# Kernel tuning notes

Hardware: AMD Instinct MI355X
Metric: run time of the kernel (lower is better)

Reference implementation:

```python
import jax, jax.numpy as jnp
import numpy as np

D_MODEL = 128
N_HEADS = 4
HEAD_DIM = D_MODEL // N_HEADS


def setup_inputs() -> dict:
    key = jax.random.key(0)
    kx, kq, ko = jax.random.split(key, 3)
    B, T = 4, 4096
    x = jax.random.normal(kx, (B, T, D_MODEL), dtype=jnp.float32)
    s = 1.0 / np.sqrt(D_MODEL)
    # torch nn.Linear weight: [out, in]; y = x @ W.T
    W_qkv = jax.random.uniform(kq, (3 * D_MODEL, D_MODEL), dtype=jnp.float32, minval=-s, maxval=s)
    W_out = jax.random.uniform(ko, (D_MODEL, D_MODEL), dtype=jnp.float32, minval=-s, maxval=s)
    return {"x": x, "W_qkv": W_qkv, "W_out": W_out}


def reference(x, W_qkv, W_out):
    B, T, _ = x.shape
    qkv = (x @ W_qkv.T).reshape(B, T, 3, N_HEADS, HEAD_DIM)
    q, k, v = qkv[:, :, 0], qkv[:, :, 1], qkv[:, :, 2]  # [B,T,H,D]
    # scores: [B,H,T,T]
    scores = jnp.einsum('bthd,bshd->bhts', q, k) / jnp.sqrt(jnp.float32(HEAD_DIM))
    causal = jnp.triu(jnp.ones((T, T), dtype=bool), 1)
    scores = jnp.where(causal, -jnp.inf, scores)
    attn = jax.nn.softmax(scores, axis=-1)
    out = jnp.einsum('bhts,bshd->bthd', attn, v).reshape(B, T, D_MODEL)
    return out @ W_out.T
```

## Files before the change

kernel.cpp:

```cpp
#include <hip/hip_runtime.h>
#include <math.h>

#define B_   4
#define T_   4096
#define DM_  128
#define NH_  4
#define HD_  32
#define TOKENS (B_ * T_)

typedef __attribute__((ext_vector_type(8))) short short8;
typedef __attribute__((ext_vector_type(4))) float floatx4;

__device__ __forceinline__ unsigned short f2bf(float f) {
    union { float f; unsigned int u; } v; v.f = f;
    unsigned int u = v.u;
    u += 0x7fffu + ((u >> 16) & 1u);
    return (unsigned short)(u >> 16);
}
__device__ __forceinline__ void split_bf(float v, unsigned short& hi, unsigned short& lo) {
    unsigned short h = f2bf(v);
    float hf = __uint_as_float(((unsigned int)h) << 16);
    hi = h;
    lo = f2bf(v - hf);
}

#define LROW 136

__global__ __launch_bounds__(256) void qkv_proj_kernel(
    const float* __restrict__ x, const float* __restrict__ Wqkv,
    unsigned short* __restrict__ q_bf, unsigned short* __restrict__ k_bf,
    unsigned short* __restrict__ v_t)
{
    __shared__ __align__(16) unsigned short whi[64 * LROW];
    __shared__ __align__(16) unsigned short wlo[64 * LROW];

    const int tid  = threadIdx.x;
    const int wave = tid >> 6, lane = tid & 63;
    const int m    = lane & 15, q4 = lane >> 4;
    const int m0   = blockIdx.x * 64;
    const int ch   = blockIdx.y;
    const float scale = 0.2550052509571414f;

    {
        const float4* wg = (const float4*)(Wqkv + (size_t)ch * 64 * DM_);
        #pragma unroll
        for (int i = 0; i < 8; ++i) {
            const int f = tid + 256 * i;
            float4 v = wg[f];
            const int row = f >> 5, k4 = f & 31;
            ushort4 h, l;
            split_bf(v.x, h.x, l.x); split_bf(v.y, h.y, l.y);
            split_bf(v.z, h.z, l.z); split_bf(v.w, h.w, l.w);
            *(ushort4*)(whi + row * LROW + k4 * 4) = h;
            *(ushort4*)(wlo + row * LROW + k4 * 4) = l;
        }
    }

    short8 Ah[4], Al[4];
    {
        const float4* xg = (const float4*)(x + (size_t)(m0 + wave * 16 + m) * DM_);
        #pragma unroll
        for (int ks = 0; ks < 4; ++ks) {
            float4 a = xg[ks * 8 + q4 * 2];
            float4 b = xg[ks * 8 + q4 * 2 + 1];
            ushort4 h0, l0, h1, l1;
            split_bf(a.x, h0.x, l0.x); split_bf(a.y, h0.y, l0.y);
            split_bf(a.z, h0.z, l0.z); split_bf(a.w, h0.w, l0.w);
            split_bf(b.x, h1.x, l1.x); split_bf(b.y, h1.y, l1.y);
            split_bf(b.z, h1.z, l1.z); split_bf(b.w, h1.w, l1.w);
            Ah[ks] = short8{(short)h0.x, (short)h0.y, (short)h0.z, (short)h0.w,
                            (short)h1.x, (short)h1.y, (short)h1.z, (short)h1.w};
            Al[ks] = short8{(short)l0.x, (short)l0.y, (short)l0.z, (short)l0.w,
                            (short)l1.x, (short)l1.y, (short)l1.z, (short)l1.w};
        }
    }
    __syncthreads();

    #pragma unroll
    for (int nb = 0; nb < 4; ++nb) {
        floatx4 acc = {0.f, 0.f, 0.f, 0.f};
        #pragma unroll
        for (int ks = 0; ks < 4; ++ks) {
            short8 Bh = *(const short8*)(whi + (nb * 16 + m) * LROW + ks * 32 + q4 * 8);
            short8 Bl = *(const short8*)(wlo + (nb * 16 + m) * LROW + ks * 32 + q4 * 8);
            acc = __builtin_amdgcn_mfma_f32_16x16x32_bf16(Ah[ks], Bh, acc, 0, 0, 0);
            acc = __builtin_amdgcn_mfma_f32_16x16x32_bf16(Ah[ks], Bl, acc, 0, 0, 0);
            acc = __builtin_amdgcn_mfma_f32_16x16x32_bf16(Al[ks], Bh, acc, 0, 0, 0);
        }
        const int n    = ch * 64 + nb * 16 + m;
        const int cidx = n >> 7;
        const int hh   = (n >> 5) & 3;
        const int d    = n & 31;
        const int tok0 = m0 + wave * 16 + q4 * 4;
        const int b    = tok0 >> 12;
        const int t0   = tok0 & (T_ - 1);
        const int bh   = b * NH_ + hh;
        if (cidx == 0) {
            #pragma unroll
            for (int reg = 0; reg < 4; ++reg)
                q_bf[((size_t)bh * T_ + t0 + reg) * HD_ + d] = f2bf(acc[reg] * scale);
        } else if (cidx == 1) {
            #pragma unroll
            for (int reg = 0; reg < 4; ++reg)
                k_bf[((size_t)bh * T_ + t0 + reg) * HD_ + d] = f2bf(acc[reg]);
        } else {
            ushort4 p;
            p.x = f2bf(acc[0]); p.y = f2bf(acc[1]);
            p.z = f2bf(acc[2]); p.w = f2bf(acc[3]);
            *(ushort4*)(v_t + ((size_t)bh * HD_ + d) * T_ + t0) = p;
        }
    }
}

__global__ __launch_bounds__(256, 4) void attn_mfma_kernel(
    const unsigned short* __restrict__ qb, const unsigned short* __restrict__ kb,
    const unsigned short* __restrict__ vtb, float* __restrict__ og)
{
    __shared__ __align__(16) char smem[5120 + 4608 + 4 * 2304];
    char* kLds = smem;
    char* vLds = smem + 5120;
    const int tid  = threadIdx.x;
    const int wave = tid >> 6, lane = tid & 63;
    const int m    = lane & 15, q4 = lane >> 4;
    char* pT = smem + 9728 + wave * 2304;

    const int pid = blockIdx.x;
    const int xcd = pid & 7;
    const int r_  = pid >> 3;
    const int bh  = xcd * 2 + (r_ & 1);
    const int j_  = r_ >> 1;
    const int a_  = j_ & 15, k_ = j_ >> 4;
    const int qt  = (k_ == 0) ? a_ : (k_ == 1) ? 63 - a_
                  : (k_ == 2) ? 32 + a_ : 31 - a_;

    const size_t qkbase = (size_t)bh * T_ * HD_;
    const char* kg = (const char*)(kb + qkbase);
    const char* vg = (const char*)(vtb + qkbase);

    short8 qf = *(const short8*)((const char*)(qb + qkbase)
                 + (size_t)(qt * 64 + wave * 16 + m) * 64 + q4 * 16);
    const int qrow = wave * 16 + m;

    floatx4 O0 = {0.f, 0.f, 0.f, 0.f}, O1 = {0.f, 0.f, 0.f, 0.f};
    float mx = -INFINITY, ls = 0.f;

    for (int kt = 0; kt <= qt; ++kt) {
        __syncthreads();
        {
            const int krow = tid >> 2, ku = tid & 3;
            short8 kv = *(const short8*)(kg + (size_t)(kt * 64 + krow) * 64 + ku * 16);
            const int vd = tid >> 3, vu = tid & 7;
            short8 vv = *(const short8*)(vg + (size_t)vd * (T_ * 2)
                                            + (size_t)kt * 128 + vu * 16);
            *(short8*)(kLds + krow * 80 + ku * 16) = kv;
            *(short8*)(vLds + vd * 144 + vu * 16) = vv;
        }
        __syncthreads();

        floatx4 st[4];
        #pragma unroll
        for (int sb = 0; sb < 4; ++sb) {
            short8 kfrag = *(const short8*)(kLds + (sb * 16 + m) * 80 + q4 * 16);
            floatx4 z = {0.f, 0.f, 0.f, 0.f};
            st[sb] = __builtin_amdgcn_mfma_f32_16x16x32_bf16(kfrag, qf, z, 0, 0, 0);
        }

        if (kt == qt) {
            #pragma unroll
            for (int sb = 0; sb < 4; ++sb)
                #pragma unroll
                for (int reg = 0; reg < 4; ++reg)
                    if (sb * 16 + q4 * 4 + reg > qrow) st[sb][reg] = -INFINITY;
        }

        float rmax = -INFINITY;
        #pragma unroll
        for (int sb = 0; sb < 4; ++sb)
            #pragma unroll
            for (int reg = 0; reg < 4; ++reg) rmax = fmaxf(rmax, st[sb][reg]);
        rmax = fmaxf(rmax, __shfl_xor(rmax, 16, 64));
        rmax = fmaxf(rmax, __shfl_xor(rmax, 32, 64));

        const float mn = fmaxf(mx, rmax);
        const float alpha = __builtin_amdgcn_exp2f(mx - mn);
        mx = mn;

        float psum = 0.f;
        #pragma unroll
        for (int sb = 0; sb < 4; ++sb) {
            float p0 = __builtin_amdgcn_exp2f(st[sb][0] - mn);
            float p1 = __builtin_amdgcn_exp2f(st[sb][1] - mn);
            float p2 = __builtin_amdgcn_exp2f(st[sb][2] - mn);
            float p3 = __builtin_amdgcn_exp2f(st[sb][3] - mn);
            psum += (p0 + p1) + (p2 + p3);
            unsigned u0 = __float_as_uint(p0) + 0x8000u;
            unsigned u1 = __float_as_uint(p1) + 0x8000u;
            unsigned u2 = __float_as_uint(p2) + 0x8000u;
            unsigned u3 = __float_as_uint(p3) + 0x8000u;
            uint2 pk;
            pk.x = __builtin_amdgcn_perm(u1, u0, 0x07060302);
            pk.y = __builtin_amdgcn_perm(u3, u2, 0x07060302);
            *(uint2*)(pT + m * 144 + sb * 32 + q4 * 8) = pk;
        }
        psum += __shfl_xor(psum, 16, 64);
        psum += __shfl_xor(psum, 32, 64);
        ls = ls * alpha + psum;
        #pragma unroll
        for (int reg = 0; reg < 4; ++reg) { O0[reg] *= alpha; O1[reg] *= alpha; }

        __asm__ volatile("s_waitcnt lgkmcnt(0)" ::: "memory");

        short8 b0  = *(const short8*)(pT + m * 144 + q4 * 16);
        short8 b1  = *(const short8*)(pT + m * 144 + 64 + q4 * 16);
        short8 v00 = *(const short8*)(vLds + m * 144 + q4 * 16);
        short8 v10 = *(const short8*)(vLds + m * 144 + 64 + q4 * 16);
        short8 v01 = *(const short8*)(vLds + (16 + m) * 144 + q4 * 16);
        short8 v11 = *(const short8*)(vLds + (16 + m) * 144 + 64 + q4 * 16);
        O0 = __builtin_amdgcn_mfma_f32_16x16x32_bf16(v00, b0, O0, 0, 0, 0);
        O0 = __builtin_amdgcn_mfma_f32_16x16x32_bf16(v10, b1, O0, 0, 0, 0);
        O1 = __builtin_amdgcn_mfma_f32_16x16x32_bf16(v01, b0, O1, 0, 0, 0);
        O1 = __builtin_amdgcn_mfma_f32_16x16x32_bf16(v11, b1, O1, 0, 0, 0);
    }

    const float inv = 1.f / ls;
    const int b = bh >> 2, h = bh & 3;
    const int t = qt * 64 + qrow;
    float* orow = og + (((size_t)b * T_ + t) * NH_ + h) * HD_;
    *(float4*)(orow + q4 * 4)      = make_float4(O0[0] * inv, O0[1] * inv,
                                                 O0[2] * inv, O0[3] * inv);
    *(float4*)(orow + 16 + q4 * 4) = make_float4(O1[0] * inv, O1[1] * inv,
                                                 O1[2] * inv, O1[3] * inv);
}

__global__ __launch_bounds__(256) void out_proj_kernel(
    const float* __restrict__ a, const float* __restrict__ Wout,
    float* __restrict__ out)
{
    __shared__ __align__(16) unsigned short whi[64 * LROW];
    __shared__ __align__(16) unsigned short wlo[64 * LROW];

    const int tid  = threadIdx.x;
    const int wave = tid >> 6, lane = tid & 63;
    const int m    = lane & 15, q4 = lane >> 4;
    const int m0   = blockIdx.x * 64;
    const int ch   = blockIdx.y;

    {
        const float4* wg = (const float4*)(Wout + (size_t)ch * 64 * DM_);
        #pragma unroll
        for (int i = 0; i < 8; ++i) {
            const int f = tid + 256 * i;
            float4 v = wg[f];
            const int row = f >> 5, k4 = f & 31;
            ushort4 h, l;
            split_bf(v.x, h.x, l.x); split_bf(v.y, h.y, l.y);
            split_bf(v.z, h.z, l.z); split_bf(v.w, h.w, l.w);
            *(ushort4*)(whi + row * LROW + k4 * 4) = h;
            *(ushort4*)(wlo + row * LROW + k4 * 4) = l;
        }
    }

    short8 Ah[4], Al[4];
    {
        const float4* xg = (const float4*)(a + (size_t)(m0 + wave * 16 + m) * DM_);
        #pragma unroll
        for (int ks = 0; ks < 4; ++ks) {
            float4 av = xg[ks * 8 + q4 * 2];
            float4 bv = xg[ks * 8 + q4 * 2 + 1];
            ushort4 h0, l0, h1, l1;
            split_bf(av.x, h0.x, l0.x); split_bf(av.y, h0.y, l0.y);
            split_bf(av.z, h0.z, l0.z); split_bf(av.w, h0.w, l0.w);
            split_bf(bv.x, h1.x, l1.x); split_bf(bv.y, h1.y, l1.y);
            split_bf(bv.z, h1.z, l1.z); split_bf(bv.w, h1.w, l1.w);
            Ah[ks] = short8{(short)h0.x, (short)h0.y, (short)h0.z, (short)h0.w,
                            (short)h1.x, (short)h1.y, (short)h1.z, (short)h1.w};
            Al[ks] = short8{(short)l0.x, (short)l0.y, (short)l0.z, (short)l0.w,
                            (short)l1.x, (short)l1.y, (short)l1.z, (short)l1.w};
        }
    }
    __syncthreads();

    #pragma unroll
    for (int nb = 0; nb < 4; ++nb) {
        floatx4 acc = {0.f, 0.f, 0.f, 0.f};
        #pragma unroll
        for (int ks = 0; ks < 4; ++ks) {
            short8 Bh = *(const short8*)(whi + (nb * 16 + m) * LROW + ks * 32 + q4 * 8);
            short8 Bl = *(const short8*)(wlo + (nb * 16 + m) * LROW + ks * 32 + q4 * 8);
            acc = __builtin_amdgcn_mfma_f32_16x16x32_bf16(Ah[ks], Bh, acc, 0, 0, 0);
            acc = __builtin_amdgcn_mfma_f32_16x16x32_bf16(Ah[ks], Bl, acc, 0, 0, 0);
            acc = __builtin_amdgcn_mfma_f32_16x16x32_bf16(Al[ks], Bh, acc, 0, 0, 0);
        }
        const int n = ch * 64 + nb * 16 + m;
        const int tok0 = m0 + wave * 16 + q4 * 4;
        #pragma unroll
        for (int reg = 0; reg < 4; ++reg)
            out[(size_t)(tok0 + reg) * DM_ + n] = acc[reg];
    }
}

extern "C" void kernel_launch(void* const* d_in, const int* in_sizes, int n_in,
                              void* d_out, int out_size, void* d_ws, size_t ws_size,
                              hipStream_t stream) {
    const float* x    = (const float*)d_in[0];
    const float* Wqkv = (const float*)d_in[1];
    const float* Wout = (const float*)d_in[2];
    float* out = (float*)d_out;

    char* ws = (char*)d_ws;
    unsigned short* q_bf  = (unsigned short*)(ws);
    unsigned short* k_bf  = (unsigned short*)(ws + (size_t)4 * 1024 * 1024);
    unsigned short* v_t   = (unsigned short*)(ws + (size_t)8 * 1024 * 1024);
    float*          att_ws = (float*)(ws + (size_t)12 * 1024 * 1024);

    qkv_proj_kernel<<<dim3(TOKENS / 64, 6), 256, 0, stream>>>(x, Wqkv, q_bf, k_bf, v_t);
    attn_mfma_kernel<<<1024, 256, 0, stream>>>(q_bf, k_bf, v_t, att_ws);
    out_proj_kernel<<<dim3(TOKENS / 64, 2), 256, 0, stream>>>(att_ws, Wout, out);
}
```

Baseline: 146.8 us.

## Give each attention wave its own 32-row query tile and drop shared K/V staging

The attention kernel now assigns each wave an independent 32-row query tile, with the four waves of a block taking mirrored tiles to balance the causal work. K and V fragments are loaded straight from global memory into registers, which removes LDS staging and the per-iteration block barriers. The row sum is computed with an extra MFMA against a ones vector instead of shuffle reductions, and the grid is halved. The V projection also swaps its MFMA operand order so V^T is written along contiguous tokens. Possible downsides are extra global/L2 traffic, since K/V are no longer shared across waves, and higher register pressure.

Result: slower. 161.4 us (+10.0%).

```diff
diff --git a/kernel.cpp b/kernel.cpp
--- a/kernel.cpp
+++ b/kernel.cpp
@@ -76,160 +76,197 @@
     }
     __syncthreads();
 
-    #pragma unroll
-    for (int nb = 0; nb < 4; ++nb) {
-        floatx4 acc = {0.f, 0.f, 0.f, 0.f};
-        #pragma unroll
-        for (int ks = 0; ks < 4; ++ks) {
-            short8 Bh = *(const short8*)(whi + (nb * 16 + m) * LROW + ks * 32 + q4 * 8);
-            short8 Bl = *(const short8*)(wlo + (nb * 16 + m) * LROW + ks * 32 + q4 * 8);
-            acc = __builtin_amdgcn_mfma_f32_16x16x32_bf16(Ah[ks], Bh, acc, 0, 0, 0);
-            acc = __builtin_amdgcn_mfma_f32_16x16x32_bf16(Ah[ks], Bl, acc, 0, 0, 0);
-            acc = __builtin_amdgcn_mfma_f32_16x16x32_bf16(Al[ks], Bh, acc, 0, 0, 0);
-        }
-        const int n    = ch * 64 + nb * 16 + m;
-        const int cidx = n >> 7;
-        const int hh   = (n >> 5) & 3;
-        const int d    = n & 31;
-        const int tok0 = m0 + wave * 16 + q4 * 4;
-        const int b    = tok0 >> 12;
-        const int t0   = tok0 & (T_ - 1);
-        const int bh   = b * NH_ + hh;
-        if (cidx == 0) {
-            #pragma unroll
-            for (int reg = 0; reg < 4; ++reg)
-                q_bf[((size_t)bh * T_ + t0 + reg) * HD_ + d] = f2bf(acc[reg] * scale);
-        } else if (cidx == 1) {
-            #pragma unroll
-            for (int reg = 0; reg < 4; ++reg)
-                k_bf[((size_t)bh * T_ + t0 + reg) * HD_ + d] = f2bf(acc[reg]);
-        } else {
-            ushort4 p;
-            p.x = f2bf(acc[0]); p.y = f2bf(acc[1]);
-            p.z = f2bf(acc[2]); p.w = f2bf(acc[3]);
-            *(ushort4*)(v_t + ((size_t)bh * HD_ + d) * T_ + t0) = p;
-        }
-    }
-}
-
-__global__ __launch_bounds__(256, 4) void attn_mfma_kernel(
+    const int b    = m0 >> 12;
+    const int tloc = (m0 & (T_ - 1)) + wave * 16;
+
+    if (ch < 4) {
+        #pragma unroll
+        for (int nb = 0; nb < 4; ++nb) {
+            floatx4 acc = {0.f, 0.f, 0.f, 0.f};
+            #pragma unroll
+            for (int ks = 0; ks < 4; ++ks) {
+                short8 Bh = *(const short8*)(whi + (nb * 16 + m) * LROW + ks * 32 + q4 * 8);
+                short8 Bl = *(const short8*)(wlo + (nb * 16 + m) * LROW + ks * 32 + q4 * 8);
+                acc = __builtin_amdgcn_mfma_f32_16x16x32_bf16(Ah[ks], Bh, acc, 0, 0, 0);
+                acc = __builtin_amdgcn_mfma_f32_16x16x32_bf16(Ah[ks], Bl, acc, 0, 0, 0);
+                acc = __builtin_amdgcn_mfma_f32_16x16x32_bf16(Al[ks], Bh, acc, 0, 0, 0);
+            }
+            const int n  = ch * 64 + nb * 16 + m;
+            const int hh = (n >> 5) & 3;
+            const int d  = n & 31;
+            const int bh = b * NH_ + hh;
+            const int t0 = tloc + q4 * 4;
+            if (ch < 2) {
+                #pragma unroll
+                for (int reg = 0; reg < 4; ++reg)
+                    q_bf[((size_t)bh * T_ + t0 + reg) * HD_ + d] = f2bf(acc[reg] * scale);
+            } else {
+                #pragma unroll
+                for (int reg = 0; reg < 4; ++reg)
+                    k_bf[((size_t)bh * T_ + t0 + reg) * HD_ + d] = f2bf(acc[reg]);
+            }
+        }
+    } else {
+        #pragma unroll
+        for (int nb = 0; nb < 4; ++nb) {
+            floatx4 acc = {0.f, 0.f, 0.f, 0.f};
+            #pragma unroll
+            for (int ks = 0; ks < 4; ++ks) {
+                short8 Bh = *(const short8*)(whi + (nb * 16 + m) * LROW + ks * 32 + q4 * 8);
+                short8 Bl = *(const short8*)(wlo + (nb * 16 + m) * LROW + ks * 32 + q4 * 8);
+                acc = __builtin_amdgcn_mfma_f32_16x16x32_bf16(Bh, Ah[ks], acc, 0, 0, 0);
+                acc = __builtin_amdgcn_mfma_f32_16x16x32_bf16(Bh, Al[ks], acc, 0, 0, 0);
+                acc = __builtin_amdgcn_mfma_f32_16x16x32_bf16(Bl, Ah[ks], acc, 0, 0, 0);
+            }
+            const int t = tloc + m;
+            #pragma unroll
+            for (int reg = 0; reg < 4; ++reg) {
+                const int n  = ch * 64 + nb * 16 + q4 * 4 + reg;
+                const int hh = (n >> 5) & 3;
+                const int d  = n & 31;
+                v_t[((size_t)(b * NH_ + hh) * HD_ + d) * T_ + t] = f2bf(acc[reg]);
+            }
+        }
+    }
+}
+
+__global__ __launch_bounds__(256) void attn_mfma_kernel(
     const unsigned short* __restrict__ qb, const unsigned short* __restrict__ kb,
     const unsigned short* __restrict__ vtb, float* __restrict__ og)
 {
-    __shared__ __align__(16) char smem[5120 + 4608 + 4 * 2304];
-    char* kLds = smem;
-    char* vLds = smem + 5120;
+    __shared__ __align__(16) char pSm[4 * 32 * 144];
     const int tid  = threadIdx.x;
     const int wave = tid >> 6, lane = tid & 63;
     const int m    = lane & 15, q4 = lane >> 4;
-    char* pT = smem + 9728 + wave * 2304;
-
-    const int pid = blockIdx.x;
-    const int xcd = pid & 7;
-    const int r_  = pid >> 3;
-    const int bh  = xcd * 2 + (r_ & 1);
-    const int j_  = r_ >> 1;
-    const int a_  = j_ & 15, k_ = j_ >> 4;
-    const int qt  = (k_ == 0) ? a_ : (k_ == 1) ? 63 - a_
-                  : (k_ == 2) ? 32 + a_ : 31 - a_;
+    char* pT = pSm + wave * 4608;
+
+    const int bidx = blockIdx.x;
+    const int xcd  = bidx & 7;
+    const int g    = bidx >> 3;
+    const int bh   = xcd * 2 + (g & 1);
+    const int u    = g >> 1;
+    const int qt   = (wave == 0) ? u : (wave == 1) ? 127 - u
+                   : (wave == 2) ? 64 + u : 63 - u;
 
     const size_t qkbase = (size_t)bh * T_ * HD_;
     const char* kg = (const char*)(kb + qkbase);
     const char* vg = (const char*)(vtb + qkbase);
-
-    short8 qf = *(const short8*)((const char*)(qb + qkbase)
-                 + (size_t)(qt * 64 + wave * 16 + m) * 64 + q4 * 16);
-    const int qrow = wave * 16 + m;
-
-    floatx4 O0 = {0.f, 0.f, 0.f, 0.f}, O1 = {0.f, 0.f, 0.f, 0.f};
-    float mx = -INFINITY, ls = 0.f;
-
-    for (int kt = 0; kt <= qt; ++kt) {
-        __syncthreads();
-        {
-            const int krow = tid >> 2, ku = tid & 3;
-            short8 kv = *(const short8*)(kg + (size_t)(kt * 64 + krow) * 64 + ku * 16);
-            const int vd = tid >> 3, vu = tid & 7;
-            short8 vv = *(const short8*)(vg + (size_t)vd * (T_ * 2)
-                                            + (size_t)kt * 128 + vu * 16);
-            *(short8*)(kLds + krow * 80 + ku * 16) = kv;
-            *(short8*)(vLds + vd * 144 + vu * 16) = vv;
-        }
-        __syncthreads();
-
-        floatx4 st[4];
-        #pragma unroll
-        for (int sb = 0; sb < 4; ++sb) {
-            short8 kfrag = *(const short8*)(kLds + (sb * 16 + m) * 80 + q4 * 16);
-            floatx4 z = {0.f, 0.f, 0.f, 0.f};
-            st[sb] = __builtin_amdgcn_mfma_f32_16x16x32_bf16(kfrag, qf, z, 0, 0, 0);
-        }
-
-        if (kt == qt) {
+    const char* qg = (const char*)(qb + qkbase);
+
+    short8 qf[2];
+    #pragma unroll
+    for (int qb_ = 0; qb_ < 2; ++qb_)
+        qf[qb_] = *(const short8*)(qg + (size_t)(qt * 32 + qb_ * 16 + m) * 64 + q4 * 16);
+
+    const short ob = (short)0x3F80;
+    const short8 onesf = (m == 0) ? short8{ob, ob, ob, ob, ob, ob, ob, ob}
+                                  : short8{0, 0, 0, 0, 0, 0, 0, 0};
+
+    floatx4 O[2][2] = {{{0.f,0.f,0.f,0.f},{0.f,0.f,0.f,0.f}},
+                       {{0.f,0.f,0.f,0.f},{0.f,0.f,0.f,0.f}}};
+    floatx4 Cs[2] = {{0.f,0.f,0.f,0.f},{0.f,0.f,0.f,0.f}};
+    float mx[2] = {-INFINITY, -INFINITY};
+
+    const int ktN = (qt * 32 + 31) >> 6;
+
+    for (int kt = 0; kt <= ktN; ++kt) {
+        short8 kf[4];
+        #pragma unroll
+        for (int sb = 0; sb < 4; ++sb)
+            kf[sb] = *(const short8*)(kg + (size_t)(kt * 64 + sb * 16 + m) * 64 + q4 * 16);
+        short8 vf[2][2];
+        #pragma unroll
+        for (int db = 0; db < 2; ++db)
+            #pragma unroll
+            for (int h = 0; h < 2; ++h)
+                vf[db][h] = *(const short8*)(vg + (size_t)(db * 16 + m) * (T_ * 2)
+                                                + kt * 128 + h * 64 + q4 * 16);
+
+        floatx4 st[4][2];
+        #pragma unroll
+        for (int sb = 0; sb < 4; ++sb)
+            #pragma unroll
+            for (int qb_ = 0; qb_ < 2; ++qb_) {
+                floatx4 z = {0.f, 0.f, 0.f, 0.f};
+                st[sb][qb_] = __builtin_amdgcn_mfma_f32_16x16x32_bf16(kf[sb], qf[qb_], z, 0, 0, 0);
+            }
+
+        if (kt == ktN) {
             #pragma unroll
             for (int sb = 0; sb < 4; ++sb)
                 #pragma unroll
-                for (int reg = 0; reg < 4; ++reg)
-                    if (sb * 16 + q4 * 4 + reg > qrow) st[sb][reg] = -INFINITY;
-        }
-
-        float rmax = -INFINITY;
-        #pragma unroll
-        for (int sb = 0; sb < 4; ++sb)
-            #pragma unroll
-            for (int reg = 0; reg < 4; ++reg) rmax = fmaxf(rmax, st[sb][reg]);
-        rmax = fmaxf(rmax, __shfl_xor(rmax, 16, 64));
-        rmax = fmaxf(rmax, __shfl_xor(rmax, 32, 64));
-
-        const float mn = fmaxf(mx, rmax);
-        const float alpha = __builtin_amdgcn_exp2f(mx - mn);
-        mx = mn;
-
-        float psum = 0.f;
-        #pragma unroll
-        for (int sb = 0; sb < 4; ++sb) {
-            float p0 = __builtin_amdgcn_exp2f(st[sb][0] - mn);
-            float p1 = __builtin_amdgcn_exp2f(st[sb][1] - mn);
-            float p2 = __builtin_amdgcn_exp2f(st[sb][2] - mn);
-            float p3 = __builtin_amdgcn_exp2f(st[sb][3] - mn);
-            psum += (p0 + p1) + (p2 + p3);
-            unsigned u0 = __float_as_uint(p0) + 0x8000u;
-            unsigned u1 = __float_as_uint(p1) + 0x8000u;
-            unsigned u2 = __float_as_uint(p2) + 0x8000u;
-            unsigned u3 = __float_as_uint(p3) + 0x8000u;
-            uint2 pk;
-            pk.x = __builtin_amdgcn_perm(u1, u0, 0x07060302);
-            pk.y = __builtin_amdgcn_perm(u3, u2, 0x07060302);
-            *(uint2*)(pT + m * 144 + sb * 32 + q4 * 8) = pk;
-        }
-        psum += __shfl_xor(psum, 16, 64);
-        psum += __shfl_xor(psum, 32, 64);
-        ls = ls * alpha + psum;
-        #pragma unroll
-        for (int reg = 0; reg < 4; ++reg) { O0[reg] *= alpha; O1[reg] *= alpha; }
+                for (int qb_ = 0; qb_ < 2; ++qb_) {
+                    const int qloc = ((qt & 1) << 5) + qb_ * 16 + m;
+                    #pragma unroll
+                    for (int reg = 0; reg < 4; ++reg)
+                        if (sb * 16 + q4 * 4 + reg > qloc) st[sb][qb_][reg] = -INFINITY;
+                }
+        }
+
+        #pragma unroll
+        for (int qb_ = 0; qb_ < 2; ++qb_) {
+            float rmax = -INFINITY;
+            #pragma unroll
+            for (int sb = 0; sb < 4; ++sb)
+                #pragma unroll
+                for (int reg = 0; reg < 4; ++reg) rmax = fmaxf(rmax, st[sb][qb_][reg]);
+            rmax = fmaxf(rmax, __shfl_xor(rmax, 16, 64));
+            rmax = fmaxf(rmax, __shfl_xor(rmax, 32, 64));
+            const float mn = fmaxf(mx[qb_], rmax);
+            const float alpha = __builtin_amdgcn_exp2f(mx[qb_] - mn);
+            mx[qb_] = mn;
+            #pragma unroll
+            for (int db = 0; db < 2; ++db)
+                #pragma unroll
+                for (int reg = 0; reg < 4; ++reg) O[db][qb_][reg] *= alpha;
+            #pragma unroll
+            for (int reg = 0; reg < 4; ++reg) Cs[qb_][reg] *= alpha;
+
+            #pragma unroll
+            for (int sb = 0; sb < 4; ++sb) {
+                float p0 = __builtin_amdgcn_exp2f(st[sb][qb_][0] - mn);
+                float p1 = __builtin_amdgcn_exp2f(st[sb][qb_][1] - mn);
+                float p2 = __builtin_amdgcn_exp2f(st[sb][qb_][2] - mn);
+                float p3 = __builtin_amdgcn_exp2f(st[sb][qb_][3] - mn);
+                unsigned u0 = __float_as_uint(p0) + 0x8000u;
+                unsigned u1 = __float_as_uint(p1) + 0x8000u;
+                unsigned u2 = __float_as_uint(p2) + 0x8000u;
+                unsigned u3 = __float_as_uint(p3) + 0x8000u;
+                uint2 pk;
+                pk.x = __builtin_amdgcn_perm(u1, u0, 0x07060302);
+                pk.y = __builtin_amdgcn_perm(u3, u2, 0x07060302);
+                *(uint2*)(pT + (qb_ * 16 + m) * 144 + sb * 32 + q4 * 8) = pk;
+            }
+        }
 
         __asm__ volatile("s_waitcnt lgkmcnt(0)" ::: "memory");
 
-        short8 b0  = *(const short8*)(pT + m * 144 + q4 * 16);
-        short8 b1  = *(const short8*)(pT + m * 144 + 64 + q4 * 16);
-        short8 v00 = *(const short8*)(vLds + m * 144 + q4 * 16);
-        short8 v10 = *(const short8*)(vLds + m * 144 + 64 + q4 * 16);
-        short8 v01 = *(const short8*)(vLds + (16 + m) * 144 + q4 * 16);
-        short8 v11 = *(const short8*)(vLds + (16 + m) * 144 + 64 + q4 * 16);
-        O0 = __builtin_amdgcn_mfma_f32_16x16x32_bf16(v00, b0, O0, 0, 0, 0);
-        O0 = __builtin_amdgcn_mfma_f32_16x16x32_bf16(v10, b1, O0, 0, 0, 0);
-        O1 = __builtin_amdgcn_mfma_f32_16x16x32_bf16(v01, b0, O1, 0, 0, 0);
-        O1 = __builtin_amdgcn_mfma_f32_16x16x32_bf16(v11, b1, O1, 0, 0, 0);
-    }
-
-    const float inv = 1.f / ls;
+        #pragma unroll
+        for (int qb_ = 0; qb_ < 2; ++qb_) {
+            short8 pf0 = *(const short8*)(pT + (qb_ * 16 + m) * 144 + q4 * 16);
+            short8 pf1 = *(const short8*)(pT + (qb_ * 16 + m) * 144 + 64 + q4 * 16);
+            O[0][qb_] = __builtin_amdgcn_mfma_f32_16x16x32_bf16(vf[0][0], pf0, O[0][qb_], 0, 0, 0);
+            O[0][qb_] = __builtin_amdgcn_mfma_f32_16x16x32_bf16(vf[0][1], pf1, O[0][qb_], 0, 0, 0);
+            O[1][qb_] = __builtin_amdgcn_mfma_f32_16x16x32_bf16(vf[1][0], pf0, O[1][qb_], 0, 0, 0);
+            O[1][qb_] = __builtin_amdgcn_mfma_f32_16x16x32_bf16(vf[1][1], pf1, O[1][qb_], 0, 0, 0);
+            Cs[qb_]   = __builtin_amdgcn_mfma_f32_16x16x32_bf16(onesf, pf0, Cs[qb_], 0, 0, 0);
+            Cs[qb_]   = __builtin_amdgcn_mfma_f32_16x16x32_bf16(onesf, pf1, Cs[qb_], 0, 0, 0);
+        }
+    }
+
     const int b = bh >> 2, h = bh & 3;
-    const int t = qt * 64 + qrow;
-    float* orow = og + (((size_t)b * T_ + t) * NH_ + h) * HD_;
-    *(float4*)(orow + q4 * 4)      = make_float4(O0[0] * inv, O0[1] * inv,
-                                                 O0[2] * inv, O0[3] * inv);
-    *(float4*)(orow + 16 + q4 * 4) = make_float4(O1[0] * inv, O1[1] * inv,
-                                                 O1[2] * inv, O1[3] * inv);
+    #pragma unroll
+    for (int qb_ = 0; qb_ < 2; ++qb_) {
+        const float l = __shfl(Cs[qb_][0], m, 64);
+        const float inv = 1.f / l;
+        const int t = qt * 32 + qb_ * 16 + m;
+        float* orow = og + (((size_t)b * T_ + t) * NH_ + h) * HD_;
+        #pragma unroll
+        for (int db = 0; db < 2; ++db)
+            *(float4*)(orow + db * 16 + q4 * 4) =
+                make_float4(O[db][qb_][0] * inv, O[db][qb_][1] * inv,
+                            O[db][qb_][2] * inv, O[db][qb_][3] * inv);
+    }
 }
 
 __global__ __launch_bounds__(256) void out_proj_kernel(
@@ -314,6 +351,6 @@
     float*          att_ws = (float*)(ws + (size_t)12 * 1024 * 1024);
 
     qkv_proj_kernel<<<dim3(TOKENS / 64, 6), 256, 0, stream>>>(x, Wqkv, q_bf, k_bf, v_t);
-    attn_mfma_kernel<<<1024, 256, 0, stream>>>(q_bf, k_bf, v_t, att_ws);
+    attn_mfma_kernel<<<512, 256, 0, stream>>>(q_bf, k_bf, v_t, att_ws);
     out_proj_kernel<<<dim3(TOKENS / 64, 2), 256, 0, stream>>>(att_ws, Wout, out);
 }
```

## Pre-split weights once and emit attention output as bf16 hi/lo pairs

Applied to the files above, without the earlier changes.

Adds a small kernel that splits both weight matrices into bf16 hi/lo parts once, so the projection kernels stop redoing the split per block through LDS and can drop the block-wide sync. The attention kernel now writes its output already split into hi/lo bf16 planes, and the output projection loads these directly instead of converting fp32. The V projection path also swaps MFMA operand order, so each lane writes tokens contiguously into the transposed V layout. The cost is an extra kernel launch and weight fragments read from global/L2 instead of LDS.

Result: slower. 171.6 us (+16.9%).

```diff
diff --git a/kernel.cpp b/kernel.cpp
--- a/kernel.cpp
+++ b/kernel.cpp
@@ -24,37 +24,36 @@
     lo = f2bf(v - hf);
 }
 
-#define LROW 136
+__global__ __launch_bounds__(256) void w_split_kernel(
+    const float* __restrict__ Wqkv, const float* __restrict__ Wout,
+    unsigned short* __restrict__ w_hi, unsigned short* __restrict__ w_lo,
+    unsigned short* __restrict__ wo_hi, unsigned short* __restrict__ wo_lo)
+{
+    const int i = blockIdx.x * 256 + threadIdx.x;
+    {
+        unsigned short h, l;
+        split_bf(Wqkv[i], h, l);
+        w_hi[i] = h; w_lo[i] = l;
+    }
+    if (i < DM_ * DM_) {
+        unsigned short h, l;
+        split_bf(Wout[i], h, l);
+        wo_hi[i] = h; wo_lo[i] = l;
+    }
+}
 
 __global__ __launch_bounds__(256) void qkv_proj_kernel(
-    const float* __restrict__ x, const float* __restrict__ Wqkv,
+    const float* __restrict__ x,
+    const unsigned short* __restrict__ w_hi, const unsigned short* __restrict__ w_lo,
     unsigned short* __restrict__ q_bf, unsigned short* __restrict__ k_bf,
     unsigned short* __restrict__ v_t)
 {
-    __shared__ __align__(16) unsigned short whi[64 * LROW];
-    __shared__ __align__(16) unsigned short wlo[64 * LROW];
-
     const int tid  = threadIdx.x;
     const int wave = tid >> 6, lane = tid & 63;
     const int m    = lane & 15, q4 = lane >> 4;
     const int m0   = blockIdx.x * 64;
     const int ch   = blockIdx.y;
     const float scale = 0.2550052509571414f;
-
-    {
-        const float4* wg = (const float4*)(Wqkv + (size_t)ch * 64 * DM_);
-        #pragma unroll
-        for (int i = 0; i < 8; ++i) {
-            const int f = tid + 256 * i;
-            float4 v = wg[f];
-            const int row = f >> 5, k4 = f & 31;
-            ushort4 h, l;
-            split_bf(v.x, h.x, l.x); split_bf(v.y, h.y, l.y);
-            split_bf(v.z, h.z, l.z); split_bf(v.w, h.w, l.w);
-            *(ushort4*)(whi + row * LROW + k4 * 4) = h;
-            *(ushort4*)(wlo + row * LROW + k4 * 4) = l;
-        }
-    }
 
     short8 Ah[4], Al[4];
     {
@@ -74,47 +73,67 @@
                             (short)l1.x, (short)l1.y, (short)l1.z, (short)l1.w};
         }
     }
-    __syncthreads();
-
-    #pragma unroll
-    for (int nb = 0; nb < 4; ++nb) {
-        floatx4 acc = {0.f, 0.f, 0.f, 0.f};
-        #pragma unroll
-        for (int ks = 0; ks < 4; ++ks) {
-            short8 Bh = *(const short8*)(whi + (nb * 16 + m) * LROW + ks * 32 + q4 * 8);
-            short8 Bl = *(const short8*)(wlo + (nb * 16 + m) * LROW + ks * 32 + q4 * 8);
-            acc = __builtin_amdgcn_mfma_f32_16x16x32_bf16(Ah[ks], Bh, acc, 0, 0, 0);
-            acc = __builtin_amdgcn_mfma_f32_16x16x32_bf16(Ah[ks], Bl, acc, 0, 0, 0);
-            acc = __builtin_amdgcn_mfma_f32_16x16x32_bf16(Al[ks], Bh, acc, 0, 0, 0);
-        }
-        const int n    = ch * 64 + nb * 16 + m;
-        const int cidx = n >> 7;
-        const int hh   = (n >> 5) & 3;
-        const int d    = n & 31;
-        const int tok0 = m0 + wave * 16 + q4 * 4;
-        const int b    = tok0 >> 12;
-        const int t0   = tok0 & (T_ - 1);
-        const int bh   = b * NH_ + hh;
-        if (cidx == 0) {
-            #pragma unroll
-            for (int reg = 0; reg < 4; ++reg)
-                q_bf[((size_t)bh * T_ + t0 + reg) * HD_ + d] = f2bf(acc[reg] * scale);
-        } else if (cidx == 1) {
-            #pragma unroll
-            for (int reg = 0; reg < 4; ++reg)
-                k_bf[((size_t)bh * T_ + t0 + reg) * HD_ + d] = f2bf(acc[reg]);
-        } else {
-            ushort4 p;
-            p.x = f2bf(acc[0]); p.y = f2bf(acc[1]);
-            p.z = f2bf(acc[2]); p.w = f2bf(acc[3]);
-            *(ushort4*)(v_t + ((size_t)bh * HD_ + d) * T_ + t0) = p;
+
+    const unsigned short* wh = w_hi + (size_t)ch * 64 * DM_;
+    const unsigned short* wl = w_lo + (size_t)ch * 64 * DM_;
+    const int b    = m0 >> 12;
+    const int tloc = (m0 & (T_ - 1)) + wave * 16;
+
+    if (ch < 4) {
+        #pragma unroll
+        for (int nb = 0; nb < 4; ++nb) {
+            floatx4 acc = {0.f, 0.f, 0.f, 0.f};
+            #pragma unroll
+            for (int ks = 0; ks < 4; ++ks) {
+                short8 Bh = *(const short8*)(wh + (nb * 16 + m) * DM_ + ks * 32 + q4 * 8);
+                short8 Bl = *(const short8*)(wl + (nb * 16 + m) * DM_ + ks * 32 + q4 * 8);
+                acc = __builtin_amdgcn_mfma_f32_16x16x32_bf16(Ah[ks], Bh, acc, 0, 0, 0);
+                acc = __builtin_amdgcn_mfma_f32_16x16x32_bf16(Ah[ks], Bl, acc, 0, 0, 0);
+                acc = __builtin_amdgcn_mfma_f32_16x16x32_bf16(Al[ks], Bh, acc, 0, 0, 0);
+            }
+            const int n  = ch * 64 + nb * 16 + m;
+            const int hh = (n >> 5) & 3;
+            const int d  = n & 31;
+            const int bh = b * NH_ + hh;
+            const int t0 = tloc + q4 * 4;
+            if (ch < 2) {
+                #pragma unroll
+                for (int reg = 0; reg < 4; ++reg)
+                    q_bf[((size_t)bh * T_ + t0 + reg) * HD_ + d] = f2bf(acc[reg] * scale);
+            } else {
+                #pragma unroll
+                for (int reg = 0; reg < 4; ++reg)
+                    k_bf[((size_t)bh * T_ + t0 + reg) * HD_ + d] = f2bf(acc[reg]);
+            }
+        }
+    } else {
+        #pragma unroll
+        for (int nb = 0; nb < 4; ++nb) {
+            floatx4 acc = {0.f, 0.f, 0.f, 0.f};
+            #pragma unroll
+            for (int ks = 0; ks < 4; ++ks) {
+                short8 Bh = *(const short8*)(wh + (nb * 16 + m) * DM_ + ks * 32 + q4 * 8);
+                short8 Bl = *(const short8*)(wl + (nb * 16 + m) * DM_ + ks * 32 + q4 * 8);
+                acc = __builtin_amdgcn_mfma_f32_16x16x32_bf16(Bh, Ah[ks], acc, 0, 0, 0);
+                acc = __builtin_amdgcn_mfma_f32_16x16x32_bf16(Bh, Al[ks], acc, 0, 0, 0);
+                acc = __builtin_amdgcn_mfma_f32_16x16x32_bf16(Bl, Ah[ks], acc, 0, 0, 0);
+            }
+            const int t = tloc + m;
+            #pragma unroll
+            for (int reg = 0; reg < 4; ++reg) {
+                const int n  = ch * 64 + nb * 16 + q4 * 4 + reg;
+                const int hh = (n >> 5) & 3;
+                const int d  = n & 31;
+                v_t[((size_t)(b * NH_ + hh) * HD_ + d) * T_ + t] = f2bf(acc[reg]);
+            }
         }
     }
 }
 
 __global__ __launch_bounds__(256, 4) void attn_mfma_kernel(
     const unsigned short* __restrict__ qb, const unsigned short* __restrict__ kb,
-    const unsigned short* __restrict__ vtb, float* __restrict__ og)
+    const unsigned short* __restrict__ vtb,
+    unsigned short* __restrict__ att_hi, unsigned short* __restrict__ att_lo)
 {
     __shared__ __align__(16) char smem[5120 + 4608 + 4 * 2304];
     char* kLds = smem;
@@ -225,68 +244,49 @@
     const float inv = 1.f / ls;
     const int b = bh >> 2, h = bh & 3;
     const int t = qt * 64 + qrow;
-    float* orow = og + (((size_t)b * T_ + t) * NH_ + h) * HD_;
-    *(float4*)(orow + q4 * 4)      = make_float4(O0[0] * inv, O0[1] * inv,
-                                                 O0[2] * inv, O0[3] * inv);
-    *(float4*)(orow + 16 + q4 * 4) = make_float4(O1[0] * inv, O1[1] * inv,
-                                                 O1[2] * inv, O1[3] * inv);
+    const size_t rowoff = (((size_t)b * T_ + t) * NH_ + h) * HD_;
+    ushort4 h0, l0, h1, l1;
+    split_bf(O0[0] * inv, h0.x, l0.x); split_bf(O0[1] * inv, h0.y, l0.y);
+    split_bf(O0[2] * inv, h0.z, l0.z); split_bf(O0[3] * inv, h0.w, l0.w);
+    split_bf(O1[0] * inv, h1.x, l1.x); split_bf(O1[1] * inv, h1.y, l1.y);
+    split_bf(O1[2] * inv, h1.z, l1.z); split_bf(O1[3] * inv, h1.w, l1.w);
+    *(ushort4*)(att_hi + rowoff + q4 * 4)      = h0;
+    *(ushort4*)(att_hi + rowoff + 16 + q4 * 4) = h1;
+    *(ushort4*)(att_lo + rowoff + q4 * 4)      = l0;
+    *(ushort4*)(att_lo + rowoff + 16 + q4 * 4) = l1;
 }
 
 __global__ __launch_bounds__(256) void out_proj_kernel(
-    const float* __restrict__ a, const float* __restrict__ Wout,
+    const unsigned short* __restrict__ att_hi, const unsigned short* __restrict__ att_lo,
+    const unsigned short* __restrict__ wo_hi, const unsigned short* __restrict__ wo_lo,
     float* __restrict__ out)
 {
-    __shared__ __align__(16) unsigned short whi[64 * LROW];
-    __shared__ __align__(16) unsigned short wlo[64 * LROW];
-
     const int tid  = threadIdx.x;
     const int wave = tid >> 6, lane = tid & 63;
     const int m    = lane & 15, q4 = lane >> 4;
     const int m0   = blockIdx.x * 64;
     const int ch   = blockIdx.y;
 
-    {
-        const float4* wg = (const float4*)(Wout + (size_t)ch * 64 * DM_);
-        #pragma unroll
-        for (int i = 0; i < 8; ++i) {
-            const int f = tid + 256 * i;
-            float4 v = wg[f];
-            const int row = f >> 5, k4 = f & 31;
-            ushort4 h, l;
-            split_bf(v.x, h.x, l.x); split_bf(v.y, h.y, l.y);
-            split_bf(v.z, h.z, l.z); split_bf(v.w, h.w, l.w);
-            *(ushort4*)(whi + row * LROW + k4 * 4) = h;
-            *(ushort4*)(wlo + row * LROW + k4 * 4) = l;
-        }
-    }
-
     short8 Ah[4], Al[4];
     {
-        const float4* xg = (const float4*)(a + (size_t)(m0 + wave * 16 + m) * DM_);
+        const size_t row = (size_t)(m0 + wave * 16 + m) * DM_;
         #pragma unroll
         for (int ks = 0; ks < 4; ++ks) {
-            float4 av = xg[ks * 8 + q4 * 2];
-            float4 bv = xg[ks * 8 + q4 * 2 + 1];
-            ushort4 h0, l0, h1, l1;
-            split_bf(av.x, h0.x, l0.x); split_bf(av.y, h0.y, l0.y);
-            split_bf(av.z, h0.z, l0.z); split_bf(av.w, h0.w, l0.w);
-            split_bf(bv.x, h1.x, l1.x); split_bf(bv.y, h1.y, l1.y);
-            split_bf(bv.z, h1.z, l1.z); split_bf(bv.w, h1.w, l1.w);
-            Ah[ks] = short8{(short)h0.x, (short)h0.y, (short)h0.z, (short)h0.w,
-                            (short)h1.x, (short)h1.y, (short)h1.z, (short)h1.w};
-            Al[ks] = short8{(short)l0.x, (short)l0.y, (short)l0.z, (short)l0.w,
-                            (short)l1.x, (short)l1.y, (short)l1.z, (short)l1.w};
-        }
-    }
-    __syncthreads();
+            Ah[ks] = *(const short8*)(att_hi + row + ks * 32 + q4 * 8);
+            Al[ks] = *(const short8*)(att_lo + row + ks * 32 + q4 * 8);
+        }
+    }
+
+    const unsigned short* wh = wo_hi + (size_t)ch * 64 * DM_;
+    const unsigned short* wl = wo_lo + (size_t)ch * 64 * DM_;
 
     #pragma unroll
     for (int nb = 0; nb < 4; ++nb) {
         floatx4 acc = {0.f, 0.f, 0.f, 0.f};
         #pragma unroll
         for (int ks = 0; ks < 4; ++ks) {
-            short8 Bh = *(const short8*)(whi + (nb * 16 + m) * LROW + ks * 32 + q4 * 8);
-            short8 Bl = *(const short8*)(wlo + (nb * 16 + m) * LROW + ks * 32 + q4 * 8);
+            short8 Bh = *(const short8*)(wh + (nb * 16 + m) * DM_ + ks * 32 + q4 * 8);
+            short8 Bl = *(const short8*)(wl + (nb * 16 + m) * DM_ + ks * 32 + q4 * 8);
             acc = __builtin_amdgcn_mfma_f32_16x16x32_bf16(Ah[ks], Bh, acc, 0, 0, 0);
             acc = __builtin_amdgcn_mfma_f32_16x16x32_bf16(Ah[ks], Bl, acc, 0, 0, 0);
             acc = __builtin_amdgcn_mfma_f32_16x16x32_bf16(Al[ks], Bh, acc, 0, 0, 0);
@@ -308,12 +308,19 @@
     float* out = (float*)d_out;
 
     char* ws = (char*)d_ws;
-    unsigned short* q_bf  = (unsigned short*)(ws);
-    unsigned short* k_bf  = (unsigned short*)(ws + (size_t)4 * 1024 * 1024);
-    unsigned short* v_t   = (unsigned short*)(ws + (size_t)8 * 1024 * 1024);
-    float*          att_ws = (float*)(ws + (size_t)12 * 1024 * 1024);
-
-    qkv_proj_kernel<<<dim3(TOKENS / 64, 6), 256, 0, stream>>>(x, Wqkv, q_bf, k_bf, v_t);
-    attn_mfma_kernel<<<1024, 256, 0, stream>>>(q_bf, k_bf, v_t, att_ws);
-    out_proj_kernel<<<dim3(TOKENS / 64, 2), 256, 0, stream>>>(att_ws, Wout, out);
-}
+    const size_t MB = 1024 * 1024;
+    unsigned short* q_bf   = (unsigned short*)(ws);
+    unsigned short* k_bf   = (unsigned short*)(ws + 4 * MB);
+    unsigned short* v_t    = (unsigned short*)(ws + 8 * MB);
+    unsigned short* att_hi = (unsigned short*)(ws + 12 * MB);
+    unsigned short* att_lo = (unsigned short*)(ws + 16 * MB);
+    unsigned short* w_hi   = (unsigned short*)(ws + 20 * MB);
+    unsigned short* w_lo   = (unsigned short*)(ws + 20 * MB + 96 * 1024);
+    unsigned short* wo_hi  = (unsigned short*)(ws + 20 * MB + 192 * 1024);
+    unsigned short* wo_lo  = (unsigned short*)(ws + 20 * MB + 224 * 1024);
+
+    w_split_kernel<<<192, 256, 0, stream>>>(Wqkv, Wout, w_hi, w_lo, wo_hi, wo_lo);
+    qkv_proj_kernel<<<dim3(TOKENS / 64, 6), 256, 0, stream>>>(x, w_hi, w_lo, q_bf, k_bf, v_t);
+    attn_mfma_kernel<<<1024, 256, 0, stream>>>(q_bf, k_bf, v_t, att_hi, att_lo);
+    out_proj_kernel<<<dim3(TOKENS / 64, 2), 256, 0, stream>>>(att_hi, att_lo, wo_hi, wo_lo, out);
+}
```
